# Performance work log

Measured on AMD Instinct MI355X. Metric: run time of the kernel, lower is better.

## Reference

```python
import jax, jax.numpy as jnp
import numpy as np

OBS, HOR, PD, HID, NH, PROTO = 8, 8, 128, 256, 8, 32
B, N = 8, 4096

def _gelu(x):
    return jax.nn.gelu(x, approximate=False)  # torch nn.GELU default is exact erf

def setup_inputs():
    key = jax.random.key(0)
    ks = iter(jax.random.split(key, 40))
    nrm = lambda shape, s=0.02: jax.random.normal(next(ks), shape, dtype=jnp.float32) * s
    return {
        'obs_points': jax.random.normal(next(ks), (B, N, OBS, 2), dtype=jnp.float32),
        'obs_vis': jax.random.randint(next(ks), (B, N, OBS), 0, 2).astype(bool),
        'rel_xy': jax.random.normal(next(ks), (B, N, 2), dtype=jnp.float32),
        'anchor_obs': jax.random.normal(next(ks), (B, OBS, 2), dtype=jnp.float32),
        'anchor_obs_vel': jax.random.normal(next(ks), (B, OBS, 2), dtype=jnp.float32),
        'semantic_feat': jax.random.normal(next(ks), (B, N, 10), dtype=jnp.float32),
        'ln_w': jnp.ones((OBS * 7,), jnp.float32),
        'ln_b': jnp.zeros((OBS * 7,), jnp.float32),
        'enc_w1': nrm((OBS * 7, PD)), 'enc_b1': jnp.zeros((PD,), jnp.float32),
        'enc_w2': nrm((PD, PD)), 'enc_b2': jnp.zeros((PD,), jnp.float32),
        'time_embed': nrm((HOR, HID)),
        'anchor_w': nrm((OBS * 4, HID)), 'anchor_b': jnp.zeros((HID,), jnp.float32),
        'query_w': nrm((PD, HID)), 'query_b': jnp.zeros((HID,), jnp.float32),
        'in_proj_w': nrm((HID, 3 * HID)), 'in_proj_b': jnp.zeros((3 * HID,), jnp.float32),
        'out_proj_w': nrm((HID, HID)), 'out_proj_b': jnp.zeros((HID,), jnp.float32),
        'ah_w': nrm((HID, 2)), 'ah_b': jnp.zeros((2,), jnp.float32),
        'rh_w1': nrm((HID + PD + 2, HID)), 'rh_b1': jnp.zeros((HID,), jnp.float32),
        'rh_w2': nrm((HID, 2)), 'rh_b2': jnp.zeros((2,), jnp.float32),
        'vh_w1': nrm((HID + PD, HID // 2)), 'vh_b1': jnp.zeros((HID // 2,), jnp.float32),
        'vh_w2': nrm((HID // 2, 1)), 'vh_b2': jnp.zeros((1,), jnp.float32),
        'sh_w': nrm((HID, PROTO)), 'sh_b': jnp.zeros((PROTO,), jnp.float32),
    }

def reference(obs_points, obs_vis, rel_xy, anchor_obs, anchor_obs_vel, semantic_feat,
              ln_w, ln_b, enc_w1, enc_b1, enc_w2, enc_b2, time_embed,
              anchor_w, anchor_b, query_w, query_b, in_proj_w, in_proj_b,
              out_proj_w, out_proj_b, ah_w, ah_b, rh_w1, rh_b1, rh_w2, rh_b2,
              vh_w1, vh_b1, vh_w2, vh_b2, sh_w, sh_b):
    del semantic_feat  # unused, matches original
    Bc, Nc, T, _ = obs_points.shape
    # ---- PointTraceEncoder ----
    vel = jnp.concatenate([jnp.zeros_like(obs_points[:, :, :1]),
                           obs_points[:, :, 1:] - obs_points[:, :, :-1]], axis=2)
    rel = jnp.broadcast_to(rel_xy[:, :, None, :], (Bc, Nc, T, 2))
    feat = jnp.concatenate([obs_points, vel, obs_vis.astype(jnp.float32)[..., None], rel],
                           axis=-1).reshape(Bc, Nc, T * 7)
    mu = feat.mean(-1, keepdims=True)
    var = ((feat - mu) ** 2).mean(-1, keepdims=True)
    x = (feat - mu) / jnp.sqrt(var + 1e-5) * ln_w + ln_b
    point_tokens = _gelu(_gelu(x @ enc_w1 + enc_b1) @ enc_w2 + enc_b2)  # [B,N,PD]
    # ---- queries / memory ----
    anchor_feat = jnp.concatenate([anchor_obs, anchor_obs_vel], -1).reshape(Bc, -1)
    tq = time_embed[None] + (anchor_feat @ anchor_w + anchor_b)[:, None]  # [B,HOR,HID]
    mem = point_tokens @ query_w + query_b  # [B,N,HID]
    # ---- multi-head cross attention ----
    D = tq.shape[-1]; dh = D // NH
    q = tq @ in_proj_w[:, :D] + in_proj_b[:D]
    k = mem @ in_proj_w[:, D:2 * D] + in_proj_b[D:2 * D]
    v = mem @ in_proj_w[:, 2 * D:] + in_proj_b[2 * D:]
    qh = q.reshape(Bc, -1, NH, dh).transpose(0, 2, 1, 3)
    kh = k.reshape(Bc, -1, NH, dh).transpose(0, 2, 1, 3)
    vh = v.reshape(Bc, -1, NH, dh).transpose(0, 2, 1, 3)
    attn = jax.nn.softmax(jnp.einsum('bhqd,bhkd->bhqk', qh, kh) / jnp.sqrt(jnp.float32(dh)), axis=-1)
    o = jnp.einsum('bhqk,bhkd->bhqd', attn, vh).transpose(0, 2, 1, 3).reshape(Bc, -1, D)
    future = o @ out_proj_w + out_proj_b  # [B,HOR,HID]
    # ---- heads ----
    last_anchor = anchor_obs[:, -1]
    anchor_delta = 0.1 * jnp.tanh(future @ ah_w + ah_b)
    anchor_pred = last_anchor[:, None] + jnp.cumsum(anchor_delta, axis=1)  # [B,HOR,2]
    Hq = future.shape[1]
    ft_e = jnp.broadcast_to(future[:, :, None, :], (Bc, Hq, Nc, D))
    pt_e = jnp.broadcast_to(point_tokens[:, None], (Bc, Hq, Nc, point_tokens.shape[-1]))
    rel_e = jnp.broadcast_to(rel_xy[:, None], (Bc, Hq, Nc, 2))
    per_point = jnp.concatenate([ft_e, pt_e, rel_e], axis=-1)  # [B,HOR,N,HID+PD+2]
    residual = 0.1 * jnp.tanh(_gelu(per_point @ rh_w1 + rh_b1) @ rh_w2 + rh_b2)
    pred_points = anchor_pred[:, :, None, :] + residual
    vis_logits = (_gelu(per_point[..., :-2] @ vh_w1 + vh_b1) @ vh_w2 + vh_b2)[..., 0]
    sem_logits = future @ sh_w + sh_b
    return (anchor_pred,
            pred_points.transpose(0, 2, 1, 3),   # [B,N,HOR,2]
            vis_logits.transpose(0, 2, 1),       # [B,N,HOR]
            sem_logits)                           # [B,HOR,PROTO]
```

## Files before the change

kernel.cpp:

```cpp
#include <hip/hip_runtime.h>
#include <math.h>

#define BB 8
#define NN 4096
#define TT 8
#define HORQ 8
#define PD 128
#define HID 256
#define NHD 8
#define DH 32
#define FE 56
#define NC2 16
#define CH2 256

typedef __attribute__((ext_vector_type(8))) short short8;
typedef __attribute__((ext_vector_type(4))) float floatx4;
typedef unsigned short ushort_t;

__device__ __forceinline__ float gelu_fast(float x) {
    float x2 = x * x;
    float y2 = x * fmaf(0.0713551f, x2, 1.5957691f);
    float e = __expf(y2);
    return x - x * __builtin_amdgcn_rcpf(1.f + e);
}

__device__ __forceinline__ float tanh_fast(float x) {
    float e = __expf(2.f * x);
    return 1.f - 2.f * __builtin_amdgcn_rcpf(1.f + e);
}

__device__ __forceinline__ ushort_t f2b(float x) {
    union { float f; unsigned u; } c; c.f = x;
    unsigned r = c.u + 0x7fffu + ((c.u >> 16) & 1u);
    return (ushort_t)(r >> 16);
}
__device__ __forceinline__ float b2f(unsigned hi) {
    union { unsigned u; float f; } c; c.u = hi;
    return c.f;
}

__global__ __launch_bounds__(256) void k_fuse(
    const float* __restrict__ qw, const float* __restrict__ qb,
    const float* __restrict__ ipw, const float* __restrict__ ipb,
    float* __restrict__ Wk, float* __restrict__ Wv,
    float* __restrict__ bk, float* __restrict__ bv)
{
    int j = threadIdx.x;
    int blk = blockIdx.x;
    if (blk < PD) {
        float sk = 0.f, sv = 0.f;
        for (int l = 0; l < HID; l++) {
            float w = qw[blk * HID + l];
            sk += w * ipw[l * 768 + 256 + j];
            sv += w * ipw[l * 768 + 512 + j];
        }
        Wk[blk * HID + j] = sk;
        Wv[blk * HID + j] = sv;
    } else {
        float sk = ipb[256 + j], sv = ipb[512 + j];
        for (int l = 0; l < HID; l++) {
            float w = qb[l];
            sk += w * ipw[l * 768 + 256 + j];
            sv += w * ipw[l * 768 + 512 + j];
        }
        bk[j] = sk;
        bv[j] = sv;
    }
}

__global__ __launch_bounds__(256) void k_prep(
    const float* __restrict__ Wk, const float* __restrict__ Wv,
    const float* __restrict__ rw1, const float* __restrict__ vw1,
    const float* __restrict__ w1, const float* __restrict__ w2,
    short* __restrict__ Wfrag, short* __restrict__ w1frag, short* __restrict__ w2frag)
{
    int tid = threadIdx.x;
    int blk = blockIdx.x;
    int ks = tid >> 6, lane = tid & 63;
    int quad = lane >> 4, c16 = lane & 15;
    if (blk < 56) {
        int nt = blk;
        int n = nt * 16 + c16;
        for (int j = 0; j < 8; j++) {
            int k = ks * 32 + quad * 8 + j;
            float v;
            if (n < 256)      v = Wk[k * HID + n];
            else if (n < 512) v = Wv[k * HID + (n - 256)];
            else if (n < 768) v = rw1[(256 + k) * HID + (n - 512)];
            else              v = vw1[(256 + k) * PD + (n - 768)];
            Wfrag[((nt * 4 + ks) * 64 + lane) * 8 + j] = (short)f2b(v);
        }
    } else if (blk < 64) {
        if (ks < 2) {
            int nt = blk - 56;
            int n = nt * 16 + c16;
            for (int j = 0; j < 8; j++) {
                int k = ks * 32 + quad * 8 + j;
                float v = (k < FE) ? w1[k * PD + n] : 0.f;
                w1frag[((nt * 2 + ks) * 64 + lane) * 8 + j] = (short)f2b(v);
            }
        }
    } else {
        int nt = blk - 64;
        int n = nt * 16 + c16;
        for (int j = 0; j < 8; j++) {
            int k = ks * 32 + quad * 8 + j;
            w2frag[((nt * 4 + ks) * 64 + lane) * 8 + j] = (short)f2b(w2[k * PD + n]);
        }
    }
}

#define U1_OFF 0
#define XNB_OFF 17408
#define PTB_OFF 26624
#define RXY_OFF 44032
#define MU_OFF 44544
#define RS_OFF 44800
#define SMEM_BYTES 45056

__global__ __launch_bounds__(256) void k_main(
    const float* __restrict__ obs, const int* __restrict__ vis,
    const float* __restrict__ rel,
    const float* __restrict__ lnw, const float* __restrict__ lnb,
    const float* __restrict__ b1, const float* __restrict__ b2,
    const short* __restrict__ Wfrag, const short* __restrict__ w1frag,
    const short* __restrict__ w2frag,
    const float* __restrict__ bk, const float* __restrict__ bv,
    const float* __restrict__ rw1,
    float* __restrict__ kb, float* __restrict__ vb,
    ushort_t* __restrict__ P1, ushort_t* __restrict__ P2)
{
    __shared__ __align__(16) char smem[SMEM_BYTES];
    float* xnf = (float*)(smem + U1_OFF);
    short* h1b = (short*)(smem + U1_OFF);
    short* xnb = (short*)(smem + XNB_OFF);
    short* ptb = (short*)(smem + PTB_OFF);
    float* rxyS = (float*)(smem + RXY_OFF);
    float* muS = (float*)(smem + MU_OFF);
    float* rsS = (float*)(smem + RS_OFF);

    int tid = threadIdx.x;
    int w = tid >> 6, lane = tid & 63;
    int quad = lane >> 4, c16 = lane & 15;
    int bn0 = blockIdx.x * 64;

    for (int idx = tid; idx < 64 * FE; idx += 256) {
        int p = idx / FE, e = idx - p * FE;
        int t = e / 7, c = e - t * 7;
        int bn = bn0 + p;
        float v;
        if (c < 2)       v = obs[(bn * TT + t) * 2 + c];
        else if (c < 4)  v = (t == 0) ? 0.f : (obs[(bn * TT + t) * 2 + (c - 2)] - obs[(bn * TT + t - 1) * 2 + (c - 2)]);
        else if (c == 4) v = (float)vis[bn * TT + t];
        else             v = rel[bn * 2 + (c - 5)];
        xnf[p * 57 + e] = v;
    }
    if (tid < 128) rxyS[tid] = rel[bn0 * 2 + tid];
    __syncthreads();

    if (tid < 64) {
        float s = 0.f, ss = 0.f;
        for (int e = 0; e < FE; e++) { float v = xnf[tid * 57 + e]; s += v; ss += v * v; }
        float mu = s * (1.f / FE);
        float var = ss * (1.f / FE) - mu * mu;
        muS[tid] = mu;
        rsS[tid] = rsqrtf(var + 1e-5f);
    }
    __syncthreads();

    for (int idx = tid; idx < 64 * 64; idx += 256) {
        int p = idx >> 6, e = idx & 63;
        float v = 0.f;
        if (e < FE) v = (xnf[p * 57 + e] - muS[p]) * rsS[p] * lnw[e] + lnb[e];
        xnb[p * 72 + e] = (short)f2b(v);
    }
    __syncthreads();

    {
        short8 af1[4][2];
        #pragma unroll
        for (int mt = 0; mt < 4; mt++)
            #pragma unroll
            for (int ks = 0; ks < 2; ks++)
                af1[mt][ks] = *(const short8*)(xnb + (mt * 16 + c16) * 72 + ks * 32 + quad * 8);
        #pragma unroll
        for (int ntl = 0; ntl < 2; ntl++) {
            int nt = w * 2 + ntl;
            short8 bf1[2];
            #pragma unroll
            for (int ks = 0; ks < 2; ks++)
                bf1[ks] = *(const short8*)(w1frag + ((nt * 2 + ks) * 64 + lane) * 8);
            int col = nt * 16 + c16;
            float bb = b1[col];
            #pragma unroll
            for (int mt = 0; mt < 4; mt++) {
                floatx4 acc = {0.f, 0.f, 0.f, 0.f};
                acc = __builtin_amdgcn_mfma_f32_16x16x32_bf16(af1[mt][0], bf1[0], acc, 0, 0, 0);
                acc = __builtin_amdgcn_mfma_f32_16x16x32_bf16(af1[mt][1], bf1[1], acc, 0, 0, 0);
                #pragma unroll
                for (int r = 0; r < 4; r++) {
                    int row = mt * 16 + quad * 4 + r;
                    h1b[row * 136 + col] = (short)f2b(gelu_fast(acc[r] + bb));
                }
            }
        }
    }
    __syncthreads();

    {
        short8 af2[4][4];
        #pragma unroll
        for (int mt = 0; mt < 4; mt++)
            #pragma unroll
            for (int ks = 0; ks < 4; ks++)
                af2[mt][ks] = *(const short8*)(h1b + (mt * 16 + c16) * 136 + ks * 32 + quad * 8);
        #pragma unroll
        for (int ntl = 0; ntl < 2; ntl++) {
            int nt = w * 2 + ntl;
            short8 bf2[4];
            #pragma unroll
            for (int ks = 0; ks < 4; ks++)
                bf2[ks] = *(const short8*)(w2frag + ((nt * 4 + ks) * 64 + lane) * 8);
            int col = nt * 16 + c16;
            float bb = b2[col];
            #pragma unroll
            for (int mt = 0; mt < 4; mt++) {
                floatx4 acc = {0.f, 0.f, 0.f, 0.f};
                #pragma unroll
                for (int ks = 0; ks < 4; ks++)
                    acc = __builtin_amdgcn_mfma_f32_16x16x32_bf16(af2[mt][ks], bf2[ks], acc, 0, 0, 0);
                #pragma unroll
                for (int r = 0; r < 4; r++) {
                    int row = mt * 16 + quad * 4 + r;
                    ptb[row * 136 + col] = (short)f2b(gelu_fast(acc[r] + bb));
                }
            }
        }
    }
    __syncthreads();

    {
        short8 af[4][4];
        #pragma unroll
        for (int mt = 0; mt < 4; mt++)
            #pragma unroll
            for (int ks = 0; ks < 4; ks++)
                af[mt][ks] = *(const short8*)(ptb + (mt * 16 + c16) * 136 + ks * 32 + quad * 8);
        for (int i = 0; i < 14; i++) {
            int nt = w + i * 4;
            short8 bf[4];
            #pragma unroll
            for (int ks = 0; ks < 4; ks++)
                bf[ks] = *(const short8*)(Wfrag + ((nt * 4 + ks) * 64 + lane) * 8);
            floatx4 acc[4];
            #pragma unroll
            for (int mt = 0; mt < 4; mt++) {
                acc[mt] = (floatx4){0.f, 0.f, 0.f, 0.f};
                #pragma unroll
                for (int ks = 0; ks < 4; ks++)
                    acc[mt] = __builtin_amdgcn_mfma_f32_16x16x32_bf16(af[mt][ks], bf[ks], acc[mt], 0, 0, 0);
            }
            int n = nt * 16 + c16;
            if (nt < 16) {
                float bb = bk[n];
                #pragma unroll
                for (int mt = 0; mt < 4; mt++)
                    #pragma unroll
                    for (int r = 0; r < 4; r++) {
                        int row = mt * 16 + quad * 4 + r;
                        kb[(size_t)(bn0 + row) * HID + n] = acc[mt][r] + bb;
                    }
            } else if (nt < 32) {
                int j = n - 256;
                float bb = bv[j];
                #pragma unroll
                for (int mt = 0; mt < 4; mt++)
                    #pragma unroll
                    for (int r = 0; r < 4; r++) {
                        int row = mt * 16 + quad * 4 + r;
                        vb[(size_t)(bn0 + row) * HID + j] = acc[mt][r] + bb;
                    }
            } else if (nt < 48) {
                int j = n - 512;
                float wr0 = rw1[384 * HID + j], wr1 = rw1[385 * HID + j];
                #pragma unroll
                for (int mt = 0; mt < 4; mt++)
                    #pragma unroll
                    for (int r = 0; r < 4; r++) {
                        int row = mt * 16 + quad * 4 + r;
                        P1[(size_t)(bn0 + row) * HID + j] =
                            f2b(acc[mt][r] + rxyS[row * 2] * wr0 + rxyS[row * 2 + 1] * wr1);
                    }
            } else {
                int j = n - 768;
                #pragma unroll
                for (int mt = 0; mt < 4; mt++)
                    #pragma unroll
                    for (int r = 0; r < 4; r++) {
                        int row = mt * 16 + quad * 4 + r;
                        P2[(size_t)(bn0 + row) * PD + j] = f2b(acc[mt][r]);
                    }
            }
        }
    }
}

__global__ __launch_bounds__(256) void k_tq(
    const float* __restrict__ aobs, const float* __restrict__ avel,
    const float* __restrict__ te, const float* __restrict__ aw, const float* __restrict__ ab,
    const float* __restrict__ ipw, const float* __restrict__ ipb,
    float* __restrict__ qb_)
{
    __shared__ float af[32];
    __shared__ float tq[HID];
    int tid = threadIdx.x;
    int b = blockIdx.x >> 3, h = blockIdx.x & 7;
    if (tid < 32) {
        int t = tid >> 2, m = tid & 3;
        af[tid] = (m < 2) ? aobs[(b * TT + t) * 2 + m] : avel[(b * TT + t) * 2 + (m - 2)];
    }
    __syncthreads();
    float s = te[h * HID + tid] + ab[tid];
    for (int i = 0; i < 32; i++) s += af[i] * aw[i * HID + tid];
    tq[tid] = s;
    __syncthreads();
    float qv = ipb[tid];
    for (int i = 0; i < HID; i++) qv += tq[i] * ipw[i * 768 + tid];
    qb_[(size_t)blockIdx.x * HID + tid] = qv;
}

__global__ __launch_bounds__(256) void k_att(
    const float* __restrict__ qbuf, const float* __restrict__ kb, const float* __restrict__ vbuf,
    float* __restrict__ pm, float* __restrict__ pl, float* __restrict__ po)
{
    __shared__ float qs[8][DH];
    __shared__ float sc[8][CH2];
    __shared__ float pos[8][8][DH];
    int tid = threadIdx.x;
    int bidx = blockIdx.x;
    int c = bidx & (NC2 - 1);
    int head = (bidx >> 4) & 7;
    int b = bidx >> 7;
    qs[tid >> 5][tid & 31] = qbuf[(size_t)(b * HORQ + (tid >> 5)) * HID + head * DH + (tid & 31)];
    __syncthreads();
    const float scale = 0.17677669529663688110f;
    {
        int nn = tid;
        int n = c * CH2 + nn;
        const float* kp = kb + (size_t)(b * NN + n) * HID + head * DH;
        float kr[DH];
        #pragma unroll
        for (int u = 0; u < DH; u += 4) {
            float4 f = *reinterpret_cast<const float4*>(kp + u);
            kr[u] = f.x; kr[u + 1] = f.y; kr[u + 2] = f.z; kr[u + 3] = f.w;
        }
        #pragma unroll
        for (int qq = 0; qq < 8; qq++) {
            float s = 0.f;
            #pragma unroll
            for (int d = 0; d < DH; d++) s += qs[qq][d] * kr[d];
            sc[qq][nn] = s * scale;
        }
    }
    __syncthreads();
    int qq = tid >> 5, r = tid & 31;
    float mx = -1e30f;
    #pragma unroll
    for (int nn = r; nn < CH2; nn += 32) mx = fmaxf(mx, sc[qq][nn]);
    #pragma unroll
    for (int m = 16; m; m >>= 1) mx = fmaxf(mx, __shfl_xor(mx, m, 32));
    float sum = 0.f;
    #pragma unroll
    for (int nn = r; nn < CH2; nn += 32) { float e = __expf(sc[qq][nn] - mx); sc[qq][nn] = e; sum += e; }
    #pragma unroll
    for (int m = 16; m; m >>= 1) sum += __shfl_xor(sum, m, 32);
    if (r == 0) { pm[bidx * 8 + qq] = mx; pl[bidx * 8 + qq] = sum; }
    __syncthreads();
    {
        int g = tid >> 5, d = tid & 31;
        float oacc[8];
        #pragma unroll
        for (int q2 = 0; q2 < 8; q2++) oacc[q2] = 0.f;
        const float* vp = vbuf + ((size_t)(b * NN + c * CH2 + g * 32)) * HID + head * DH + d;
        for (int i = 0; i < 32; i++) {
            float v = vp[(size_t)i * HID];
            int nn = g * 32 + i;
            #pragma unroll
            for (int q2 = 0; q2 < 8; q2++) oacc[q2] += sc[q2][nn] * v;
        }
        #pragma unroll
        for (int q2 = 0; q2 < 8; q2++) pos[g][q2][d] = oacc[q2];
    }
    __syncthreads();
    {
        int q2 = tid >> 5, d = tid & 31;
        float o = 0.f;
        #pragma unroll
        for (int gg = 0; gg < 8; gg++) o += pos[gg][q2][d];
        po[(size_t)(bidx * 8 + q2) * DH + d] = o;
    }
}

__global__ __launch_bounds__(256) void k_attc(
    const float* __restrict__ pm, const float* __restrict__ pl, const float* __restrict__ po,
    float* __restrict__ ob)
{
    int tid = threadIdx.x;
    int bh = blockIdx.x;
    int b = bh >> 3, head = bh & 7;
    int qq = tid >> 5, d = tid & 31;
    float M = -1e30f;
    for (int c = 0; c < NC2; c++) M = fmaxf(M, pm[(bh * NC2 + c) * 8 + qq]);
    float L = 0.f, o = 0.f;
    for (int c = 0; c < NC2; c++) {
        float w = __expf(pm[(bh * NC2 + c) * 8 + qq] - M);
        L += w * pl[(bh * NC2 + c) * 8 + qq];
        o += w * po[(size_t)((bh * NC2 + c) * 8 + qq) * DH + d];
    }
    ob[(size_t)(b * HORQ + qq) * HID + head * DH + d] = o / L;
}

__global__ __launch_bounds__(256) void k_fut(
    const float* __restrict__ ob, const float* __restrict__ opw, const float* __restrict__ opb,
    const float* __restrict__ rw1, const float* __restrict__ rb1,
    const float* __restrict__ vw1, const float* __restrict__ vb1,
    const float* __restrict__ shw, const float* __restrict__ shb,
    const float* __restrict__ ahw, const float* __restrict__ ahb,
    float* __restrict__ F1, float* __restrict__ F2, float* __restrict__ dl, float* __restrict__ sem)
{
    __shared__ float orow[HID], fut[HID];
    int tid = threadIdx.x;
    int bh = blockIdx.x;
    orow[tid] = ob[(size_t)bh * HID + tid];
    __syncthreads();
    float s = opb[tid];
    for (int i = 0; i < HID; i++) s += orow[i] * opw[i * HID + tid];
    fut[tid] = s;
    __syncthreads();
    float f1 = rb1[tid];
    for (int i = 0; i < HID; i++) f1 += fut[i] * rw1[i * HID + tid];
    F1[(size_t)bh * HID + tid] = f1;
    if (tid < PD) {
        float f2 = vb1[tid];
        for (int i = 0; i < HID; i++) f2 += fut[i] * vw1[i * PD + tid];
        F2[(size_t)bh * PD + tid] = f2;
    }
    if (tid < 32) {
        float s3 = shb[tid];
        for (int i = 0; i < HID; i++) s3 += fut[i] * shw[i * 32 + tid];
        sem[bh * 32 + tid] = s3;
    }
    if (tid < 2) {
        float a = ahb[tid];
        for (int i = 0; i < HID; i++) a += fut[i] * ahw[i * 2 + tid];
        dl[bh * 2 + tid] = 0.1f * tanhf(a);
    }
}

__global__ void k_cum(const float* __restrict__ aobs, const float* __restrict__ dl, float* __restrict__ out0)
{
    int tid = threadIdx.x;
    if (tid < 16) {
        int b = tid >> 1, c = tid & 1;
        float acc = aobs[(b * TT + 7) * 2 + c];
        for (int h = 0; h < HORQ; h++) {
            acc += dl[(b * HORQ + h) * 2 + c];
            out0[(b * HORQ + h) * 2 + c] = acc;
        }
    }
}

__global__ __launch_bounds__(256) void k_fin(
    const float* __restrict__ F1, const float* __restrict__ F2,
    const ushort_t* __restrict__ P1, const ushort_t* __restrict__ P2,
    const float* __restrict__ rw2, const float* __restrict__ rb2,
    const float* __restrict__ vw2, const float* __restrict__ vb2,
    const float* __restrict__ ap,
    float* __restrict__ out1, float* __restrict__ out2)
{
    int tile = blockIdx.x >> 1;
    int hh = blockIdx.x & 1;
    int h0 = hh * 4;
    int bn = tile * 256 + threadIdx.x;
    int b = bn >> 12;

    const uint4* p1v = (const uint4*)(P1 + (size_t)bn * HID);
    const uint4* p2v = (const uint4*)(P2 + (size_t)bn * PD);
    const float* f1base = F1 + (size_t)(b * HORQ + h0) * HID;
    const float* f2base = F2 + (size_t)(b * HORQ + h0) * PD;

    float acc0[4], acc1[4], accv[4];
    #pragma unroll
    for (int hi = 0; hi < 4; hi++) { acc0[hi] = 0.f; acc1[hi] = 0.f; accv[hi] = 0.f; }

    for (int c = 0; c < 32; c++) {
        uint4 q = p1v[c];
        unsigned wd[4] = {q.x, q.y, q.z, q.w};
        float p1f[8];
        #pragma unroll
        for (int u = 0; u < 4; u++) {
            p1f[2 * u]     = b2f(wd[u] << 16);
            p1f[2 * u + 1] = b2f(wd[u] & 0xffff0000u);
        }
        float w0[8], w1[8];
        #pragma unroll
        for (int u = 0; u < 8; u++) {
            int j = c * 8 + u;
            w0[u] = rw2[j * 2];
            w1[u] = rw2[j * 2 + 1];
        }
        #pragma unroll
        for (int hi = 0; hi < 4; hi++) {
            const float* f1p = f1base + hi * HID + c * 8;
            #pragma unroll
            for (int u = 0; u < 8; u++) {
                float g = gelu_fast(f1p[u] + p1f[u]);
                acc0[hi] += g * w0[u];
                acc1[hi] += g * w1[u];
            }
        }
    }
    for (int c = 0; c < 16; c++) {
        uint4 q = p2v[c];
        unsigned wd[4] = {q.x, q.y, q.z, q.w};
        float p2f[8];
        #pragma unroll
        for (int u = 0; u < 4; u++) {
            p2f[2 * u]     = b2f(wd[u] << 16);
            p2f[2 * u + 1] = b2f(wd[u] & 0xffff0000u);
        }
        float wv[8];
        #pragma unroll
        for (int u = 0; u < 8; u++) wv[u] = vw2[c * 8 + u];
        #pragma unroll
        for (int hi = 0; hi < 4; hi++) {
            const float* f2p = f2base + hi * PD + c * 8;
            #pragma unroll
            for (int u = 0; u < 8; u++) {
                float g = gelu_fast(f2p[u] + p2f[u]);
                accv[hi] += g * wv[u];
            }
        }
    }

    float rb20 = rb2[0], rb21 = rb2[1], vb20 = vb2[0];
    float o1[8], o2[4];
    #pragma unroll
    for (int hi = 0; hi < 4; hi++) {
        int h = h0 + hi;
        float rx = 0.1f * tanh_fast(acc0[hi] + rb20);
        float ry = 0.1f * tanh_fast(acc1[hi] + rb21);
        o1[2 * hi]     = ap[(b * HORQ + h) * 2 + 0] + rx;
        o1[2 * hi + 1] = ap[(b * HORQ + h) * 2 + 1] + ry;
        o2[hi] = accv[hi] + vb20;
    }
    float4* o1p = (float4*)(out1 + ((size_t)bn * HORQ + h0) * 2);
    o1p[0] = make_float4(o1[0], o1[1], o1[2], o1[3]);
    o1p[1] = make_float4(o1[4], o1[5], o1[6], o1[7]);
    *(float4*)(out2 + (size_t)bn * HORQ + h0) = make_float4(o2[0], o2[1], o2[2], o2[3]);
}

extern "C" void kernel_launch(void* const* d_in, const int* in_sizes, int n_in,
                              void* d_out, int out_size, void* d_ws, size_t ws_size,
                              hipStream_t stream)
{
    const float* obs  = (const float*)d_in[0];
    const int*   vis  = (const int*)d_in[1];
    const float* rel  = (const float*)d_in[2];
    const float* aobs = (const float*)d_in[3];
    const float* avel = (const float*)d_in[4];
    const float* lnw = (const float*)d_in[6];
    const float* lnb = (const float*)d_in[7];
    const float* ew1 = (const float*)d_in[8];
    const float* eb1 = (const float*)d_in[9];
    const float* ew2 = (const float*)d_in[10];
    const float* eb2 = (const float*)d_in[11];
    const float* te  = (const float*)d_in[12];
    const float* aw  = (const float*)d_in[13];
    const float* ab  = (const float*)d_in[14];
    const float* qw  = (const float*)d_in[15];
    const float* qbias = (const float*)d_in[16];
    const float* ipw = (const float*)d_in[17];
    const float* ipb = (const float*)d_in[18];
    const float* opw = (const float*)d_in[19];
    const float* opb = (const float*)d_in[20];
    const float* ahw = (const float*)d_in[21];
    const float* ahb = (const float*)d_in[22];
    const float* rw1 = (const float*)d_in[23];
    const float* rb1 = (const float*)d_in[24];
    const float* rw2 = (const float*)d_in[25];
    const float* rb2 = (const float*)d_in[26];
    const float* vw1 = (const float*)d_in[27];
    const float* vb1 = (const float*)d_in[28];
    const float* vw2 = (const float*)d_in[29];
    const float* vb2 = (const float*)d_in[30];
    const float* shw = (const float*)d_in[31];
    const float* shb = (const float*)d_in[32];

    float* W = (float*)d_ws;
    size_t o = 0;
    float* Wk  = W + o; o += (size_t)PD * HID;
    float* Wv  = W + o; o += (size_t)PD * HID;
    float* bk  = W + o; o += HID;
    float* bv  = W + o; o += HID;
    float* qb_ = W + o; o += (size_t)BB * HORQ * HID;
    float* F1  = W + o; o += (size_t)BB * HORQ * HID;
    float* F2  = W + o; o += (size_t)BB * HORQ * PD;
    float* dl  = W + o; o += (size_t)BB * HORQ * 2;
    float* ob  = W + o; o += (size_t)BB * HORQ * HID;
    float* pm  = W + o; o += (size_t)BB * NHD * NC2 * 8;
    float* pl  = W + o; o += (size_t)BB * NHD * NC2 * 8;
    float* po  = W + o; o += (size_t)BB * NHD * NC2 * 8 * DH;
    float* kb  = W + o; o += (size_t)BB * NN * HID;
    float* vbuf= W + o; o += (size_t)BB * NN * HID;
    ushort_t* P1 = (ushort_t*)(W + o); o += (size_t)BB * NN * HID / 2;
    ushort_t* P2 = (ushort_t*)(W + o); o += (size_t)BB * NN * PD / 2;
    short* Sf = (short*)(W + o);
    short* Wfrag  = Sf;
    short* w1frag = Sf + 114688;
    short* w2frag = Sf + 114688 + 8192;

    float* out0 = (float*)d_out;
    float* out1 = out0 + BB * HORQ * 2;
    float* out2 = out1 + (size_t)BB * NN * HORQ * 2;
    float* out3 = out2 + (size_t)BB * NN * HORQ;

    k_fuse<<<PD + 1, 256, 0, stream>>>(qw, qbias, ipw, ipb, Wk, Wv, bk, bv);
    k_prep<<<72, 256, 0, stream>>>(Wk, Wv, rw1, vw1, ew1, ew2, Wfrag, w1frag, w2frag);
    k_main<<<BB * NN / 64, 256, 0, stream>>>(obs, vis, rel, lnw, lnb, eb1, eb2,
                                             Wfrag, w1frag, w2frag, bk, bv, rw1,
                                             kb, vbuf, P1, P2);
    k_tq<<<BB * HORQ, 256, 0, stream>>>(aobs, avel, te, aw, ab, ipw, ipb, qb_);
    k_att<<<BB * NHD * NC2, 256, 0, stream>>>(qb_, kb, vbuf, pm, pl, po);
    k_attc<<<BB * NHD, 256, 0, stream>>>(pm, pl, po, ob);
    k_fut<<<BB * HORQ, 256, 0, stream>>>(ob, opw, opb, rw1, rb1, vw1, vb1, shw, shb, ahw, ahb,
                                         F1, F2, dl, out3);
    k_cum<<<1, 64, 0, stream>>>(aobs, dl, out0);
    k_fin<<<(BB * NN / 256) * 2, 256, 0, stream>>>(F1, F2, P1, P2, rw2, rb2, vw2, vb2,
                                                   out0, out1, out2);
}
```

Baseline: 290.3 us.

## Merge prep, query and attention-combine kernels; split final head kernel per horizon

Folds the K/V weight fusion, fragment packing, bias fusion and time-query projection into one prep kernel. It also merges the attention partial-combine into the future-projection kernel, removing three launches and the Wk/Wv/ob intermediates. The final per-point head kernel now handles one horizon per block instead of four, giving four times as many blocks for parallelism. The cost is that each block re-reads the bf16 P1/P2 tiles per horizon and writes outputs as scalar stores instead of float4 stores. The prep kernel also recomputes each fused K/V weight element with a 256-long dot product per fragment entry.

```diff
diff --git a/kernel.cpp b/kernel.cpp
--- a/kernel.cpp
+++ b/kernel.cpp
@@ -39,43 +39,20 @@
     return c.f;
 }
 
-__global__ __launch_bounds__(256) void k_fuse(
+__global__ __launch_bounds__(256) void k_prep2(
     const float* __restrict__ qw, const float* __restrict__ qb,
     const float* __restrict__ ipw, const float* __restrict__ ipb,
-    float* __restrict__ Wk, float* __restrict__ Wv,
-    float* __restrict__ bk, float* __restrict__ bv)
-{
-    int j = threadIdx.x;
-    int blk = blockIdx.x;
-    if (blk < PD) {
-        float sk = 0.f, sv = 0.f;
-        for (int l = 0; l < HID; l++) {
-            float w = qw[blk * HID + l];
-            sk += w * ipw[l * 768 + 256 + j];
-            sv += w * ipw[l * 768 + 512 + j];
-        }
-        Wk[blk * HID + j] = sk;
-        Wv[blk * HID + j] = sv;
-    } else {
-        float sk = ipb[256 + j], sv = ipb[512 + j];
-        for (int l = 0; l < HID; l++) {
-            float w = qb[l];
-            sk += w * ipw[l * 768 + 256 + j];
-            sv += w * ipw[l * 768 + 512 + j];
-        }
-        bk[j] = sk;
-        bv[j] = sv;
-    }
-}
-
-__global__ __launch_bounds__(256) void k_prep(
-    const float* __restrict__ Wk, const float* __restrict__ Wv,
     const float* __restrict__ rw1, const float* __restrict__ vw1,
     const float* __restrict__ w1, const float* __restrict__ w2,
-    short* __restrict__ Wfrag, short* __restrict__ w1frag, short* __restrict__ w2frag)
-{
+    const float* __restrict__ aobs, const float* __restrict__ avel,
+    const float* __restrict__ te, const float* __restrict__ aw, const float* __restrict__ ab,
+    short* __restrict__ Wfrag, short* __restrict__ w1frag, short* __restrict__ w2frag,
+    float* __restrict__ bk, float* __restrict__ bv, float* __restrict__ qb_)
+{
+    __shared__ float af[32];
+    __shared__ float tq[HID];
+    int blk = blockIdx.x;
     int tid = threadIdx.x;
-    int blk = blockIdx.x;
     int ks = tid >> 6, lane = tid & 63;
     int quad = lane >> 4, c16 = lane & 15;
     if (blk < 56) {
@@ -84,10 +61,16 @@
         for (int j = 0; j < 8; j++) {
             int k = ks * 32 + quad * 8 + j;
             float v;
-            if (n < 256)      v = Wk[k * HID + n];
-            else if (n < 512) v = Wv[k * HID + (n - 256)];
-            else if (n < 768) v = rw1[(256 + k) * HID + (n - 512)];
-            else              v = vw1[(256 + k) * PD + (n - 768)];
+            if (n < 512) {
+                int col = (n < 256) ? (256 + n) : (256 + n);
+                float s = 0.f;
+                for (int l = 0; l < HID; l++) s += qw[k * HID + l] * ipw[l * 768 + col];
+                v = s;
+            } else if (n < 768) {
+                v = rw1[(256 + k) * HID + (n - 512)];
+            } else {
+                v = vw1[(256 + k) * PD + (n - 768)];
+            }
             Wfrag[((nt * 4 + ks) * 64 + lane) * 8 + j] = (short)f2b(v);
         }
     } else if (blk < 64) {
@@ -100,13 +83,38 @@
                 w1frag[((nt * 2 + ks) * 64 + lane) * 8 + j] = (short)f2b(v);
             }
         }
-    } else {
+    } else if (blk < 72) {
         int nt = blk - 64;
         int n = nt * 16 + c16;
         for (int j = 0; j < 8; j++) {
             int k = ks * 32 + quad * 8 + j;
             w2frag[((nt * 4 + ks) * 64 + lane) * 8 + j] = (short)f2b(w2[k * PD + n]);
         }
+    } else if (blk == 72) {
+        int j = tid;
+        float sk = ipb[256 + j], sv = ipb[512 + j];
+        for (int l = 0; l < HID; l++) {
+            float w = qb[l];
+            sk += w * ipw[l * 768 + 256 + j];
+            sv += w * ipw[l * 768 + 512 + j];
+        }
+        bk[j] = sk;
+        bv[j] = sv;
+    } else {
+        int bh = blk - 73;
+        int b = bh >> 3, h = bh & 7;
+        if (tid < 32) {
+            int t = tid >> 2, m = tid & 3;
+            af[tid] = (m < 2) ? aobs[(b * TT + t) * 2 + m] : avel[(b * TT + t) * 2 + (m - 2)];
+        }
+        __syncthreads();
+        float s = te[h * HID + tid] + ab[tid];
+        for (int i = 0; i < 32; i++) s += af[i] * aw[i * HID + tid];
+        tq[tid] = s;
+        __syncthreads();
+        float qv = ipb[tid];
+        for (int i = 0; i < HID; i++) qv += tq[i] * ipw[i * 768 + tid];
+        qb_[(size_t)bh * HID + tid] = qv;
     }
 }
 
@@ -303,30 +311,6 @@
             }
         }
     }
-}
-
-__global__ __launch_bounds__(256) void k_tq(
-    const float* __restrict__ aobs, const float* __restrict__ avel,
-    const float* __restrict__ te, const float* __restrict__ aw, const float* __restrict__ ab,
-    const float* __restrict__ ipw, const float* __restrict__ ipb,
-    float* __restrict__ qb_)
-{
-    __shared__ float af[32];
-    __shared__ float tq[HID];
-    int tid = threadIdx.x;
-    int b = blockIdx.x >> 3, h = blockIdx.x & 7;
-    if (tid < 32) {
-        int t = tid >> 2, m = tid & 3;
-        af[tid] = (m < 2) ? aobs[(b * TT + t) * 2 + m] : avel[(b * TT + t) * 2 + (m - 2)];
-    }
-    __syncthreads();
-    float s = te[h * HID + tid] + ab[tid];
-    for (int i = 0; i < 32; i++) s += af[i] * aw[i * HID + tid];
-    tq[tid] = s;
-    __syncthreads();
-    float qv = ipb[tid];
-    for (int i = 0; i < HID; i++) qv += tq[i] * ipw[i * 768 + tid];
-    qb_[(size_t)blockIdx.x * HID + tid] = qv;
 }
 
 __global__ __launch_bounds__(256) void k_att(
@@ -401,27 +385,9 @@
     }
 }
 
-__global__ __launch_bounds__(256) void k_attc(
+__global__ __launch_bounds__(256) void k_attfut(
     const float* __restrict__ pm, const float* __restrict__ pl, const float* __restrict__ po,
-    float* __restrict__ ob)
-{
-    int tid = threadIdx.x;
-    int bh = blockIdx.x;
-    int b = bh >> 3, head = bh & 7;
-    int qq = tid >> 5, d = tid & 31;
-    float M = -1e30f;
-    for (int c = 0; c < NC2; c++) M = fmaxf(M, pm[(bh * NC2 + c) * 8 + qq]);
-    float L = 0.f, o = 0.f;
-    for (int c = 0; c < NC2; c++) {
-        float w = __expf(pm[(bh * NC2 + c) * 8 + qq] - M);
-        L += w * pl[(bh * NC2 + c) * 8 + qq];
-        o += w * po[(size_t)((bh * NC2 + c) * 8 + qq) * DH + d];
-    }
-    ob[(size_t)(b * HORQ + qq) * HID + head * DH + d] = o / L;
-}
-
-__global__ __launch_bounds__(256) void k_fut(
-    const float* __restrict__ ob, const float* __restrict__ opw, const float* __restrict__ opb,
+    const float* __restrict__ opw, const float* __restrict__ opb,
     const float* __restrict__ rw1, const float* __restrict__ rb1,
     const float* __restrict__ vw1, const float* __restrict__ vb1,
     const float* __restrict__ shw, const float* __restrict__ shb,
@@ -430,13 +396,28 @@
 {
     __shared__ float orow[HID], fut[HID];
     int tid = threadIdx.x;
-    int bh = blockIdx.x;
-    orow[tid] = ob[(size_t)bh * HID + tid];
+    int b = blockIdx.x >> 3, qq = blockIdx.x & 7;
+    {
+        int head = tid >> 5, d = tid & 31;
+        int base = b * 1024 + head * 128 + qq;
+        float M = -1e30f;
+        #pragma unroll
+        for (int c = 0; c < NC2; c++) M = fmaxf(M, pm[base + c * 8]);
+        float L = 0.f, o = 0.f;
+        #pragma unroll
+        for (int c = 0; c < NC2; c++) {
+            float wgt = __expf(pm[base + c * 8] - M);
+            L += wgt * pl[base + c * 8];
+            o += wgt * po[(size_t)(base + c * 8) * DH + d];
+        }
+        orow[head * DH + d] = o / L;
+    }
     __syncthreads();
     float s = opb[tid];
     for (int i = 0; i < HID; i++) s += orow[i] * opw[i * HID + tid];
     fut[tid] = s;
     __syncthreads();
+    int bh = b * HORQ + qq;
     float f1 = rb1[tid];
     for (int i = 0; i < HID; i++) f1 += fut[i] * rw1[i * HID + tid];
     F1[(size_t)bh * HID + tid] = f1;
@@ -478,86 +459,51 @@
     const float* __restrict__ ap,
     float* __restrict__ out1, float* __restrict__ out2)
 {
-    int tile = blockIdx.x >> 1;
-    int hh = blockIdx.x & 1;
-    int h0 = hh * 4;
+    int tile = blockIdx.x >> 3;
+    int h = blockIdx.x & 7;
     int bn = tile * 256 + threadIdx.x;
-    int b = bn >> 12;
-
+    int b = __builtin_amdgcn_readfirstlane(bn >> 12);
+    int bh = __builtin_amdgcn_readfirstlane(b * HORQ + h);
+
+    const float* f1p = F1 + (size_t)bh * HID;
+    const float* f2p = F2 + (size_t)bh * PD;
     const uint4* p1v = (const uint4*)(P1 + (size_t)bn * HID);
     const uint4* p2v = (const uint4*)(P2 + (size_t)bn * PD);
-    const float* f1base = F1 + (size_t)(b * HORQ + h0) * HID;
-    const float* f2base = F2 + (size_t)(b * HORQ + h0) * PD;
-
-    float acc0[4], acc1[4], accv[4];
-    #pragma unroll
-    for (int hi = 0; hi < 4; hi++) { acc0[hi] = 0.f; acc1[hi] = 0.f; accv[hi] = 0.f; }
-
+
+    float acc0 = 0.f, acc1 = 0.f, accv = 0.f;
     for (int c = 0; c < 32; c++) {
         uint4 q = p1v[c];
         unsigned wd[4] = {q.x, q.y, q.z, q.w};
-        float p1f[8];
         #pragma unroll
         for (int u = 0; u < 4; u++) {
-            p1f[2 * u]     = b2f(wd[u] << 16);
-            p1f[2 * u + 1] = b2f(wd[u] & 0xffff0000u);
-        }
-        float w0[8], w1[8];
-        #pragma unroll
-        for (int u = 0; u < 8; u++) {
-            int j = c * 8 + u;
-            w0[u] = rw2[j * 2];
-            w1[u] = rw2[j * 2 + 1];
-        }
-        #pragma unroll
-        for (int hi = 0; hi < 4; hi++) {
-            const float* f1p = f1base + hi * HID + c * 8;
-            #pragma unroll
-            for (int u = 0; u < 8; u++) {
-                float g = gelu_fast(f1p[u] + p1f[u]);
-                acc0[hi] += g * w0[u];
-                acc1[hi] += g * w1[u];
-            }
+            float pa = b2f(wd[u] << 16);
+            float pb = b2f(wd[u] & 0xffff0000u);
+            int j0 = c * 8 + 2 * u;
+            float ga = gelu_fast(f1p[j0] + pa);
+            float gb = gelu_fast(f1p[j0 + 1] + pb);
+            acc0 += ga * rw2[j0 * 2]     + gb * rw2[(j0 + 1) * 2];
+            acc1 += ga * rw2[j0 * 2 + 1] + gb * rw2[(j0 + 1) * 2 + 1];
         }
     }
     for (int c = 0; c < 16; c++) {
         uint4 q = p2v[c];
         unsigned wd[4] = {q.x, q.y, q.z, q.w};
-        float p2f[8];
         #pragma unroll
         for (int u = 0; u < 4; u++) {
-            p2f[2 * u]     = b2f(wd[u] << 16);
-            p2f[2 * u + 1] = b2f(wd[u] & 0xffff0000u);
-        }
-        float wv[8];
-        #pragma unroll
-        for (int u = 0; u < 8; u++) wv[u] = vw2[c * 8 + u];
-        #pragma unroll
-        for (int hi = 0; hi < 4; hi++) {
-            const float* f2p = f2base + hi * PD + c * 8;
-            #pragma unroll
-            for (int u = 0; u < 8; u++) {
-                float g = gelu_fast(f2p[u] + p2f[u]);
-                accv[hi] += g * wv[u];
-            }
-        }
-    }
-
-    float rb20 = rb2[0], rb21 = rb2[1], vb20 = vb2[0];
-    float o1[8], o2[4];
-    #pragma unroll
-    for (int hi = 0; hi < 4; hi++) {
-        int h = h0 + hi;
-        float rx = 0.1f * tanh_fast(acc0[hi] + rb20);
-        float ry = 0.1f * tanh_fast(acc1[hi] + rb21);
-        o1[2 * hi]     = ap[(b * HORQ + h) * 2 + 0] + rx;
-        o1[2 * hi + 1] = ap[(b * HORQ + h) * 2 + 1] + ry;
-        o2[hi] = accv[hi] + vb20;
-    }
-    float4* o1p = (float4*)(out1 + ((size_t)bn * HORQ + h0) * 2);
-    o1p[0] = make_float4(o1[0], o1[1], o1[2], o1[3]);
-    o1p[1] = make_float4(o1[4], o1[5], o1[6], o1[7]);
-    *(float4*)(out2 + (size_t)bn * HORQ + h0) = make_float4(o2[0], o2[1], o2[2], o2[3]);
+            float pa = b2f(wd[u] << 16);
+            float pb = b2f(wd[u] & 0xffff0000u);
+            int j0 = c * 8 + 2 * u;
+            accv += gelu_fast(f2p[j0] + pa) * vw2[j0]
+                  + gelu_fast(f2p[j0 + 1] + pb) * vw2[j0 + 1];
+        }
+    }
+
+    float rx = 0.1f * tanh_fast(acc0 + rb2[0]);
+    float ry = 0.1f * tanh_fast(acc1 + rb2[1]);
+    float ap0 = ap[bh * 2], ap1 = ap[bh * 2 + 1];
+    out1[((size_t)bn * HORQ + h) * 2 + 0] = ap0 + rx;
+    out1[((size_t)bn * HORQ + h) * 2 + 1] = ap1 + ry;
+    out2[(size_t)bn * HORQ + h] = accv + vb2[0];
 }
 
 extern "C" void kernel_launch(void* const* d_in, const int* in_sizes, int n_in,
@@ -599,15 +545,12 @@
 
     float* W = (float*)d_ws;
     size_t o = 0;
-    float* Wk  = W + o; o += (size_t)PD * HID;
-    float* Wv  = W + o; o += (size_t)PD * HID;
     float* bk  = W + o; o += HID;
     float* bv  = W + o; o += HID;
     float* qb_ = W + o; o += (size_t)BB * HORQ * HID;
     float* F1  = W + o; o += (size_t)BB * HORQ * HID;
     float* F2  = W + o; o += (size_t)BB * HORQ * PD;
     float* dl  = W + o; o += (size_t)BB * HORQ * 2;
-    float* ob  = W + o; o += (size_t)BB * HORQ * HID;
     float* pm  = W + o; o += (size_t)BB * NHD * NC2 * 8;
     float* pl  = W + o; o += (size_t)BB * NHD * NC2 * 8;
     float* po  = W + o; o += (size_t)BB * NHD * NC2 * 8 * DH;
@@ -625,17 +568,16 @@
     float* out2 = out1 + (size_t)BB * NN * HORQ * 2;
     float* out3 = out2 + (size_t)BB * NN * HORQ;
 
-    k_fuse<<<PD + 1, 256, 0, stream>>>(qw, qbias, ipw, ipb, Wk, Wv, bk, bv);
-    k_prep<<<72, 256, 0, stream>>>(Wk, Wv, rw1, vw1, ew1, ew2, Wfrag, w1frag, w2frag);
+    k_prep2<<<137, 256, 0, stream>>>(qw, qbias, ipw, ipb, rw1, vw1, ew1, ew2,
+                                     aobs, avel, te, aw, ab,
+                                     Wfrag, w1frag, w2frag, bk, bv, qb_);
     k_main<<<BB * NN / 64, 256, 0, stream>>>(obs, vis, rel, lnw, lnb, eb1, eb2,
                                              Wfrag, w1frag, w2frag, bk, bv, rw1,
                                              kb, vbuf, P1, P2);
-    k_tq<<<BB * HORQ, 256, 0, stream>>>(aobs, avel, te, aw, ab, ipw, ipb, qb_);
     k_att<<<BB * NHD * NC2, 256, 0, stream>>>(qb_, kb, vbuf, pm, pl, po);
-    k_attc<<<BB * NHD, 256, 0, stream>>>(pm, pl, po, ob);
-    k_fut<<<BB * HORQ, 256, 0, stream>>>(ob, opw, opb, rw1, rb1, vw1, vb1, shw, shb, ahw, ahb,
-                                         F1, F2, dl, out3);
+    k_attfut<<<BB * HORQ, 256, 0, stream>>>(pm, pl, po, opw, opb, rw1, rb1, vw1, vb1,
+                                            shw, shb, ahw, ahb, F1, F2, dl, out3);
     k_cum<<<1, 64, 0, stream>>>(aobs, dl, out0);
-    k_fin<<<(BB * NN / 256) * 2, 256, 0, stream>>>(F1, F2, P1, P2, rw2, rb2, vw2, vb2,
+    k_fin<<<(BB * NN / 256) * 8, 256, 0, stream>>>(F1, F2, P1, P2, rw2, rb2, vw2, vb2,
                                                    out0, out1, out2);
 }
```

Result: slower. 367.7 us (+26.6%).
